# Optimization experiments

Measured on AMD Instinct MI355X. Metric: run time of the kernel, lower is better.

## Reference

```python
import jax, jax.numpy as jnp
import numpy as np

N_INST = 8  # max instance id; ids 1..N_INST, 0 = background
MESH_NORM = 1024.0  # from SegmantationLoss._meshgrid


def _meshgrid(H, W):
    y = jnp.arange(H, dtype=jnp.float32) / MESH_NORM
    x = jnp.arange(W, dtype=jnp.float32) / MESH_NORM
    return jnp.stack([jnp.broadcast_to(y[:, None], (H, W)),
                      jnp.broadcast_to(x[None, :], (H, W))], axis=0)  # [2,H,W]


def _lovasz_hinge_batch(logits, labels, delta=1.0):
    """logits, labels: [K,P] float. Returns [K] lovasz hinge losses."""
    signs = 2.0 * labels - 1.0
    errors = delta - logits * signs
    order = jnp.argsort(-errors, axis=1)  # descending
    es = jnp.take_along_axis(errors, order, axis=1)
    gs = jnp.take_along_axis(labels, order, axis=1)
    gts = gs.sum(axis=1, keepdims=True)
    intersection = gts - jnp.cumsum(gs, axis=1)
    union = gts + jnp.cumsum(1.0 - gs, axis=1)
    jac = 1.0 - intersection / union
    grad = jnp.concatenate([jac[:, :1], jac[:, 1:] - jac[:, :-1]], axis=1)
    return (jax.nn.relu(es) * grad).sum(axis=1)


def setup_inputs() -> dict:
    key = jax.random.key(0)
    k1, k2, k3, k4 = jax.random.split(key, 4)
    B, H, W = 4, 512, 1024
    x_vec = jax.random.normal(k1, (B, 2, H, W), dtype=jnp.float32)
    # small scale so psigma = exp(10*ppsigma) stays in a sane range
    x_sigma = jax.random.normal(k2, (B, 2, H, W), dtype=jnp.float32) * 0.03
    x_seed = jax.random.normal(k3, (B, 1, H, W), dtype=jnp.float32)
    t = jax.random.randint(k4, (B, H, W), 0, 9, dtype=jnp.int32)
    return {"x_vec": x_vec, "x_sigma": x_sigma, "x_seed": x_seed, "t": t}


def reference(x_vec, x_sigma, x_seed, t):
    B, _, H, W = x_vec.shape
    mesh = _meshgrid(H, W)

    emb = jnp.tanh(x_vec) + mesh[None]          # [B,2,H,W] spatial embedding
    ppsig = x_sigma                              # [B,2,H,W] pre-pseudo-sigma
    seed = jax.nn.sigmoid(x_seed)[:, 0]          # [B,H,W]

    ids = jnp.arange(1, N_INST + 1, dtype=t.dtype)
    mf = (t[None] == ids[:, None, None, None]).astype(jnp.float32)  # [N,B,H,W]
    cnt = mf.sum(axis=(2, 3))                    # [N,B]
    present = cnt > 0
    safe = jnp.maximum(cnt, 1.0)
    n_present = jnp.maximum(present.sum(axis=0).astype(jnp.float32), 1.0)  # [B]

    # per-instance masked means
    centroid = jnp.einsum('nbhw,bchw->nbc', mf, emb) / safe[..., None]    # [N,B,2]
    inst_pps = jnp.einsum('nbhw,bchw->nbc', mf, ppsig) / safe[..., None]  # [N,B,2]
    psigma = jnp.exp(10.0 * inst_pps)                                     # [N,B,2]

    # gaussian between pixel and instance embedding (l22n)
    diff2 = (emb[None] - centroid[..., None, None]) ** 2                  # [N,B,2,H,W]
    dist = (diff2 * psigma[..., None, None]).sum(axis=2)                  # [N,B,H,W]
    gauss = jnp.exp(-0.5 * dist)                                          # [N,B,H,W]

    # lovasz hinge per instance on logits 2*gauss - 1 over all pixels
    P = H * W
    lov = _lovasz_hinge_batch((2.0 * gauss - 1.0).reshape(N_INST * B, P),
                              mf.reshape(N_INST * B, P)).reshape(N_INST, B)
    lov = jnp.where(present, lov, 0.0)
    lovasz_loss = (lov.sum(axis=0) / n_present).mean()

    # sigma loss: pixel ppsigma -> detached instance mean ppsigma
    sd = (ppsig[None] - jax.lax.stop_gradient(inst_pps)[..., None, None]) ** 2
    sl = (sd.sum(axis=2) * mf).sum(axis=(2, 3)) / safe                    # [N,B]
    sl = jnp.where(present, sl, 0.0)
    sigma_loss = (sl.sum(axis=0) / n_present).mean()

    # seed loss: background -> 0, foreground -> detached gaussian
    bg = (t == 0).astype(jnp.float32)                                     # [B,H,W]
    bg_cnt = jnp.maximum(bg.sum(axis=(1, 2)), 1.0)
    bg_loss = ((seed ** 2) * bg).sum(axis=(1, 2)) / bg_cnt                # [B]
    fg = ((seed[None] - jax.lax.stop_gradient(gauss)) ** 2 * mf).sum(axis=(2, 3)) / safe
    fg = jnp.where(present, fg, 0.0)
    seed_loss = ((bg_loss + fg.sum(axis=0)) /
                 (1.0 + present.sum(axis=0).astype(jnp.float32))).mean()

    return lovasz_loss + sigma_loss + seed_loss
```

## Files before the change

kernel.cpp:

```cpp
#include <hip/hip_runtime.h>
#include <math.h>

#define B 4
#define H 512
#define W 1024
#define P (H*W)
#define NI 8
#define NSEG 32
#define NB 512
#define INV_BW ((float)NB/2.0f)
#define NSTRIP 256
#define STRIP_PX (P/NSTRIP)
#define K1B 128
#define K1PX (P/K1B)

#define D_CENY 0
#define D_CENX 32
#define D_PSY  64
#define D_PSX  96
#define D_CNT  128
#define D_SL   160
#define D_K4C  192
#define OFF_FGP 256
#define OFF_HIST (256 + 9*1024)
#define OFF_FOLD (OFF_HIST + NSEG*NSTRIP*NB)
#define OFF_PK1  OFF_HIST

__device__ __forceinline__ float fast_tanh(float x) {
    float e = __expf(2.0f * x);
    return 1.0f - 2.0f / (e + 1.0f);
}
__device__ __forceinline__ float fast_sigmoid(float x) {
    return 1.0f / (1.0f + __expf(-x));
}
template<int CTRL, int RM>
__device__ __forceinline__ float dpp_add(float x) {
    int y = __builtin_amdgcn_update_dpp(0, __float_as_int(x), CTRL, RM, 0xF, true);
    return x + __int_as_float(y);
}
__device__ __forceinline__ float wred(float x) {
    x = dpp_add<0x111, 0xF>(x);
    x = dpp_add<0x112, 0xF>(x);
    x = dpp_add<0x114, 0xF>(x);
    x = dpp_add<0x118, 0xF>(x);
    x = dpp_add<0x142, 0xA>(x);
    x = dpp_add<0x143, 0xC>(x);
    return x;
}

__global__ __launch_bounds__(256) void k1_stats(const float* __restrict__ xv,
                                                const float* __restrict__ xs,
                                                const int*  __restrict__ t,
                                                float* __restrict__ pk1) {
    const int b = blockIdx.y, bx = blockIdx.x, tid = threadIdx.x;
    const int lane = tid & 63, wid = tid >> 6;
    const float* xv_y = xv + (size_t)b*2*P;
    const float* xv_x = xv_y + P;
    const float* xs_y = xs + (size_t)b*2*P;
    const float* xs_x = xs_y + P;
    const int*   tb   = t + (size_t)b*P;

    float cnt[NI], sey[NI], sex[NI], sgy[NI], sgx[NI], sq[NI];
    #pragma unroll
    for (int n = 0; n < NI; ++n) { cnt[n]=0.f; sey[n]=0.f; sex[n]=0.f; sgy[n]=0.f; sgx[n]=0.f; sq[n]=0.f; }

    #pragma unroll
    for (int it = 0; it < 4; ++it) {
        int p0 = bx*K1PX + it*1024 + tid*4;
        float4 vy = *(const float4*)(xv_y + p0);
        float4 vx = *(const float4*)(xv_x + p0);
        float4 sy = *(const float4*)(xs_y + p0);
        float4 sx = *(const float4*)(xs_x + p0);
        int4   tt = *(const int4*)(tb + p0);
        #pragma unroll
        for (int j = 0; j < 4; ++j) {
            int pix = p0 + j;
            float ey = fast_tanh((&vy.x)[j]) + (float)(pix >> 10) * (1.0f/1024.0f);
            float ex = fast_tanh((&vx.x)[j]) + (float)(pix & 1023) * (1.0f/1024.0f);
            float gy = (&sy.x)[j], gx = (&sx.x)[j];
            int tv = (&tt.x)[j];
            float q = gy*gy + gx*gx;
            #pragma unroll
            for (int n = 0; n < NI; ++n) {
                float m = (tv == n+1) ? 1.0f : 0.0f;
                cnt[n] += m; sey[n] += m*ey; sex[n] += m*ex;
                sgy[n] += m*gy; sgx[n] += m*gx; sq[n] += m*q;
            }
        }
    }
    __shared__ float sw[4*64];
    #define RED48(val, slot) { float r_ = wred(val); if (lane == 63) sw[wid*64 + (slot)] = r_; }
    #pragma unroll
    for (int n = 0; n < NI; ++n) {
        RED48(cnt[n], n*6+0); RED48(sey[n], n*6+1); RED48(sex[n], n*6+2);
        RED48(sgy[n], n*6+3); RED48(sgx[n], n*6+4); RED48(sq[n],  n*6+5);
    }
    #undef RED48
    __syncthreads();
    if (tid < 48) {
        float s = sw[tid] + sw[64+tid] + sw[128+tid] + sw[192+tid];
        pk1[(size_t)(b*K1B + bx)*64 + tid] = s;
    }
}

__global__ __launch_bounds__(1024) void k2_finalize(float* __restrict__ wsf,
                                                    const float* __restrict__ pk1,
                                                    float* __restrict__ out) {
    const int tid = threadIdx.x;
    __shared__ float part[16*64];
    __shared__ float ssum[4*64];
    const int v = tid & 63, g = tid >> 6;
    const int b = g >> 2, c = g & 3;
    float acc = 0.f;
    const int jbase = b*K1B + c*32;
    #pragma unroll 8
    for (int i = 0; i < 32; ++i) acc += pk1[(size_t)(jbase + i)*64 + v];
    part[g*64 + v] = acc;
    __syncthreads();
    if (tid < 256) {
        int vb = tid & 63, bb = tid >> 6;
        ssum[bb*64+vb] = part[(bb*4+0)*64+vb] + part[(bb*4+1)*64+vb]
                       + part[(bb*4+2)*64+vb] + part[(bb*4+3)*64+vb];
    }
    __syncthreads();
    if (tid < NSEG) {
        int n = tid >> 2, bb = tid & 3;
        float cv  = ssum[bb*64 + n*6+0];
        float sey = ssum[bb*64 + n*6+1];
        float sex = ssum[bb*64 + n*6+2];
        float sgy = ssum[bb*64 + n*6+3];
        float sgx = ssum[bb*64 + n*6+4];
        float sq  = ssum[bb*64 + n*6+5];
        float safe = fmaxf(cv, 1.0f);
        float ipy = sgy/safe, ipx = sgx/safe;
        wsf[D_CENY+tid] = sey/safe;
        wsf[D_CENX+tid] = sex/safe;
        wsf[D_PSY+tid]  = expf(10.0f*ipy);
        wsf[D_PSX+tid]  = expf(10.0f*ipx);
        wsf[D_CNT+tid]  = cv;
        wsf[D_SL+tid]   = sq/safe - (ipy*ipy + ipx*ipx);
    } else if (tid < 64) {
        ((unsigned*)wsf)[D_K4C + (tid - 32)] = 0u;
    } else if (tid == 64) {
        out[0] = 0.f;
    }
}

__global__ __launch_bounds__(512) void k3_hist(const float* __restrict__ xv,
                                               const float* __restrict__ xseed,
                                               const int*  __restrict__ t,
                                               const float* __restrict__ wsf,
                                               unsigned* __restrict__ hist_g,
                                               float* __restrict__ fgp) {
    const int strip = blockIdx.x;
    const int b     = blockIdx.y;
    const int tid   = threadIdx.x;
    const int lane  = tid & 63;

    __shared__ unsigned hist[NI*NB];
    {
        uint4 z = {0u,0u,0u,0u};
        #pragma unroll
        for (int i = 0; i < 2; ++i) *((uint4*)hist + i*512 + tid) = z;
    }
    __shared__ float spar[4*NI];
    if (tid < 4*NI) {
        int n = tid & (NI-1), q = tid >> 3;
        spar[tid] = wsf[q*32 + n*B + b];
    }
    __syncthreads();

    float ceny[NI], cenx[NI], psy[NI], psx[NI], fgn[NI];
    #pragma unroll
    for (int n = 0; n < NI; ++n) {
        ceny[n] = spar[n]; cenx[n] = spar[NI+n];
        psy[n] = spar[2*NI+n]; psx[n] = spar[3*NI+n];
        fgn[n] = 0.f;
    }
    float bgq = 0.f;

    const float* xv_y = xv + (size_t)b*2*P;
    const float* xv_x = xv_y + P;
    const float* sdp  = xseed + (size_t)b*P;
    const int*   tb   = t + (size_t)b*P;

    {
        int p0 = strip * STRIP_PX + tid*4;
        float4 vy = *(const float4*)(xv_y + p0);
        float4 vx = *(const float4*)(xv_x + p0);
        float4 se = *(const float4*)(sdp + p0);
        int4   tt = *(const int4*)(tb + p0);
        #pragma unroll
        for (int j = 0; j < 4; ++j) {
            int pix = p0 + j;
            float ey = fast_tanh((&vy.x)[j]) + (float)(pix >> 10) * (1.0f/1024.0f);
            float ex = fast_tanh((&vx.x)[j]) + (float)(pix & 1023) * (1.0f/1024.0f);
            int tv = (&tt.x)[j];
            float gown = 0.f;
            #pragma unroll
            for (int n = 0; n < NI; ++n) {
                float dy = ey - ceny[n], dx = ex - cenx[n];
                float g = __expf(-0.5f * (psy[n]*dy*dy + psx[n]*dx*dx));
                bool lab = (tv == n+1);
                float err = lab ? (2.0f - 2.0f*g) : (2.0f*g);
                int key = (int)(err * INV_BW);
                key = key > (NB-1) ? (NB-1) : key;
                if (key > 0) atomicAdd(&hist[n*NB + key], lab ? 0x10000u : 1u);
                if (lab) gown = g;
            }
            float s = fast_sigmoid((&se.x)[j]);
            if (tv > 0) {
                float d = s - gown;
                float dd = d*d;
                #pragma unroll
                for (int n = 0; n < NI; ++n) fgn[n] += (tv == n+1) ? dd : 0.f;
            } else {
                bgq += s*s;
            }
        }
    }
    __syncthreads();
    #pragma unroll
    for (int i = 0; i < 2; ++i) {
        int lin = i*2048 + tid*4;
        int n = lin >> 9, key = lin & (NB-1);
        uint4 v = *(const uint4*)&hist[lin];
        *(uint4*)&hist_g[((size_t)((n*4 + b)*NSTRIP + strip))*NB + key] = v;
    }
    __shared__ float sfg[NI+1];
    if (tid < NI+1) sfg[tid] = 0.f;
    __syncthreads();
    #pragma unroll
    for (int n = 0; n < NI; ++n) {
        float r = wred(fgn[n]);
        if (lane == 63 && r != 0.f) atomicAdd(&sfg[n], r);
    }
    {
        float r = wred(bgq);
        if (lane == 63) atomicAdd(&sfg[NI], r);
    }
    __syncthreads();
    if (tid < NI+1) fgp[tid*1024 + b*NSTRIP + strip] = sfg[tid];
}

__global__ __launch_bounds__(256) void k4_fused(const unsigned* __restrict__ hist_g,
                                                unsigned* __restrict__ fold,
                                                float* __restrict__ wsf,
                                                const float* __restrict__ fgp,
                                                float* __restrict__ out) {
    const int q = blockIdx.x;
    const int seg = blockIdx.y;
    const int tid = threadIdx.x;

    #pragma unroll
    for (int h = 0; h < 2; ++h) {
        int key = h*256 + tid;
        const unsigned* src = hist_g + (size_t)(seg*NSTRIP + q*64)*NB + key;
        unsigned pos = 0u, neg = 0u;
        #pragma unroll 8
        for (int s = 0; s < 64; ++s) {
            unsigned v = src[(size_t)s*NB];
            pos += v >> 16; neg += v & 0xffffu;
        }
        fold[((size_t)q*NSEG + seg)*NB + key] = pos;
        fold[(size_t)4*NSEG*NB + ((size_t)q*NSEG + seg)*NB + key] = neg;
    }

    __shared__ unsigned slast;
    __syncthreads();
    if (tid == 0) {
        __threadfence();
        unsigned* cnt4 = (unsigned*)wsf + D_K4C;
        slast = __hip_atomic_fetch_add(&cnt4[seg], 1u, __ATOMIC_ACQ_REL,
                                       __HIP_MEMORY_SCOPE_AGENT);
    }
    __syncthreads();
    if (slast != 3u) return;
    __threadfence();

    const int n = seg >> 2, b = seg & 3;
    __shared__ float scnt[NSEG];
    __shared__ float sfr[256];
    __shared__ unsigned up[256], un[256];
    __shared__ double sdd[256];
    if (tid < NSEG) scnt[tid] = wsf[D_CNT + tid];
    __syncthreads();

    if (n == 0) {
        sfr[tid] = fgp[NI*1024 + b*NSTRIP + tid];
        __syncthreads();
        #pragma unroll
        for (int d = 128; d > 0; d >>= 1) {
            if (tid < d) sfr[tid] += sfr[tid + d];
            __syncthreads();
        }
        if (tid == 0) {
            float bgs = sfr[0];
            int np = 0; float ss = 0.f, csum = 0.f;
            for (int k = 0; k < NI; ++k) {
                float cv = scnt[k*4 + b];
                csum += cv;
                if (cv > 0.5f) { np++; ss += wsf[D_SL + k*4 + b]; }
            }
            float bgc = fmaxf((float)P - csum, 1.0f);
            float bgl = bgs / bgc;
            float npf = fmaxf((float)np, 1.0f);
            atomicAdd(out, (ss/npf + bgl/(1.0f + (float)np)) * (1.0f/(float)B));
        }
        __syncthreads();
    }

    const float G = scnt[seg];
    if (G < 0.5f) return;
    int npc = 0;
    #pragma unroll
    for (int k = 0; k < NI; ++k) npc += (scnt[k*4 + b] > 0.5f) ? 1 : 0;

    sfr[tid] = fgp[n*1024 + b*NSTRIP + tid];
    __syncthreads();
    #pragma unroll
    for (int d = 128; d > 0; d >>= 1) {
        if (tid < d) sfr[tid] += sfr[tid + d];
        __syncthreads();
    }
    const float FG = sfr[0];

    unsigned pos2[2] = {0u,0u}, neg2[2] = {0u,0u};
    #pragma unroll
    for (int qq = 0; qq < 4; ++qq) {
        uint2 pv = *((const uint2*)(fold + ((size_t)qq*NSEG + seg)*NB) + tid);
        uint2 nv = *((const uint2*)(fold + (size_t)4*NSEG*NB + ((size_t)qq*NSEG + seg)*NB) + tid);
        pos2[0] += pv.x; pos2[1] += pv.y;
        neg2[0] += nv.x; neg2[1] += nv.y;
    }
    unsigned tp = pos2[0] + pos2[1];
    unsigned tn = neg2[0] + neg2[1];

    up[tid] = tp; un[tid] = tn;
    __syncthreads();
    for (int d = 1; d < 256; d <<= 1) {
        unsigned ap = (tid + d < 256) ? up[tid + d] : 0u;
        unsigned an = (tid + d < 256) ? un[tid + d] : 0u;
        __syncthreads();
        up[tid] += ap; un[tid] += an;
        __syncthreads();
    }
    const unsigned TP = up[0], TN = un[0];
    const unsigned Gu = (unsigned)(G + 0.5f);
    const unsigned NEGu = (unsigned)P - Gu;
    unsigned cump = up[tid] - tp;
    unsigned cumn = un[tid] - tn;

    const double dG = (double)G;
    double acc = 0.0;
    #pragma unroll
    for (int j = 1; j >= 0; --j) {
        unsigned cp = pos2[j], cn = neg2[j];
        int key = tid*2 + j;
        if (tid == 0 && j == 0) { cp = Gu - TP; cn = NEGu - TN; }
        if (cp | cn) {
            unsigned ep = cump, en = cumn;
            unsigned epi = ep + cp, eni = en + cn;
            double jb = 1.0 - (dG - (double)ep)  / (dG + (double)en);
            double ja = 1.0 - (dG - (double)epi) / (dG + (double)eni);
            acc += (((double)key + 0.5) * (2.0/(double)NB)) * (ja - jb);
        }
        cump += cp; cumn += cn;
    }
    sdd[tid] = acc;
    __syncthreads();
    #pragma unroll
    for (int d = 128; d > 0; d >>= 1) {
        if (tid < d) sdd[tid] += sdd[tid + d];
        __syncthreads();
    }
    if (tid == 0) {
        float npf = fmaxf((float)npc, 1.0f);
        float val = (float)sdd[0] / (npf * (float)B)
                  + (FG / G) / ((1.0f + (float)npc) * (float)B);
        atomicAdd(out, val);
    }
}

extern "C" void kernel_launch(void* const* d_in, const int* in_sizes, int n_in,
                              void* d_out, int out_size, void* d_ws, size_t ws_size,
                              hipStream_t stream) {
    (void)in_sizes; (void)n_in; (void)out_size; (void)ws_size;
    const float* xv  = (const float*)d_in[0];
    const float* xs  = (const float*)d_in[1];
    const float* xsd = (const float*)d_in[2];
    const int*   t   = (const int*)d_in[3];
    float* wsf = (float*)d_ws;
    unsigned* hist_g = (unsigned*)d_ws + OFF_HIST;
    unsigned* fold   = (unsigned*)d_ws + OFF_FOLD;
    float* pk1 = wsf + OFF_PK1;
    float* fgp = wsf + OFF_FGP;
    float* out = (float*)d_out;

    k1_stats<<<dim3(K1B, B), 256, 0, stream>>>(xv, xs, t, pk1);
    k2_finalize<<<1, 1024, 0, stream>>>(wsf, pk1, out);
    k3_hist<<<dim3(NSTRIP, B), 512, 0, stream>>>(xv, xsd, t, wsf, hist_g, fgp);
    k4_fused<<<dim3(4, NSEG), 256, 0, stream>>>(hist_g, fold, wsf, fgp, out);
}
```

Measured before the change: 132.9 us.

## Halve Lovasz histogram bins and spread stats kernel over more blocks

Reduces the error histogram from 512 to 256 bins, which halves shared-memory zeroing, global histogram writes and the fold traffic, and lets each thread own exactly one bin in the final scan. It also splits the first statistics kernel into four times as many blocks, each handling one float4 group per thread, to raise parallelism, and moves the partials buffer to its own workspace region. The final segment block reuses its own folded counts from registers. The coarser binning lowers the resolution of the Lovasz approximation, which may change the loss value slightly.

```diff
diff --git a/kernel.cpp b/kernel.cpp
--- a/kernel.cpp
+++ b/kernel.cpp
@@ -7,11 +7,11 @@
 #define P (H*W)
 #define NI 8
 #define NSEG 32
-#define NB 512
+#define NB 256
 #define INV_BW ((float)NB/2.0f)
 #define NSTRIP 256
 #define STRIP_PX (P/NSTRIP)
-#define K1B 128
+#define K1B 512
 #define K1PX (P/K1B)
 
 #define D_CENY 0
@@ -22,9 +22,9 @@
 #define D_SL   160
 #define D_K4C  192
 #define OFF_FGP 256
-#define OFF_HIST (256 + 9*1024)
+#define OFF_HIST (OFF_FGP + 9*1024)
 #define OFF_FOLD (OFF_HIST + NSEG*NSTRIP*NB)
-#define OFF_PK1  OFF_HIST
+#define OFF_PK1  (OFF_FOLD + 8*NSEG*NB)
 
 __device__ __forceinline__ float fast_tanh(float x) {
     float e = __expf(2.0f * x);
@@ -64,28 +64,25 @@
     #pragma unroll
     for (int n = 0; n < NI; ++n) { cnt[n]=0.f; sey[n]=0.f; sex[n]=0.f; sgy[n]=0.f; sgx[n]=0.f; sq[n]=0.f; }
 
-    #pragma unroll
-    for (int it = 0; it < 4; ++it) {
-        int p0 = bx*K1PX + it*1024 + tid*4;
-        float4 vy = *(const float4*)(xv_y + p0);
-        float4 vx = *(const float4*)(xv_x + p0);
-        float4 sy = *(const float4*)(xs_y + p0);
-        float4 sx = *(const float4*)(xs_x + p0);
-        int4   tt = *(const int4*)(tb + p0);
+    int p0 = bx*K1PX + tid*4;
+    float4 vy = *(const float4*)(xv_y + p0);
+    float4 vx = *(const float4*)(xv_x + p0);
+    float4 sy = *(const float4*)(xs_y + p0);
+    float4 sx = *(const float4*)(xs_x + p0);
+    int4   tt = *(const int4*)(tb + p0);
+    #pragma unroll
+    for (int j = 0; j < 4; ++j) {
+        int pix = p0 + j;
+        float ey = fast_tanh((&vy.x)[j]) + (float)(pix >> 10) * (1.0f/1024.0f);
+        float ex = fast_tanh((&vx.x)[j]) + (float)(pix & 1023) * (1.0f/1024.0f);
+        float gy = (&sy.x)[j], gx = (&sx.x)[j];
+        int tv = (&tt.x)[j];
+        float q = gy*gy + gx*gx;
         #pragma unroll
-        for (int j = 0; j < 4; ++j) {
-            int pix = p0 + j;
-            float ey = fast_tanh((&vy.x)[j]) + (float)(pix >> 10) * (1.0f/1024.0f);
-            float ex = fast_tanh((&vx.x)[j]) + (float)(pix & 1023) * (1.0f/1024.0f);
-            float gy = (&sy.x)[j], gx = (&sx.x)[j];
-            int tv = (&tt.x)[j];
-            float q = gy*gy + gx*gx;
-            #pragma unroll
-            for (int n = 0; n < NI; ++n) {
-                float m = (tv == n+1) ? 1.0f : 0.0f;
-                cnt[n] += m; sey[n] += m*ey; sex[n] += m*ex;
-                sgy[n] += m*gy; sgx[n] += m*gx; sq[n] += m*q;
-            }
+        for (int n = 0; n < NI; ++n) {
+            float m = (tv == n+1) ? 1.0f : 0.0f;
+            cnt[n] += m; sey[n] += m*ey; sex[n] += m*ex;
+            sgy[n] += m*gy; sgx[n] += m*gx; sq[n] += m*q;
         }
     }
     __shared__ float sw[4*64];
@@ -112,9 +109,9 @@
     const int v = tid & 63, g = tid >> 6;
     const int b = g >> 2, c = g & 3;
     float acc = 0.f;
-    const int jbase = b*K1B + c*32;
+    const int jbase = b*K1B + c*128;
     #pragma unroll 8
-    for (int i = 0; i < 32; ++i) acc += pk1[(size_t)(jbase + i)*64 + v];
+    for (int i = 0; i < 128; ++i) acc += pk1[(size_t)(jbase + i)*64 + v];
     part[g*64 + v] = acc;
     __syncthreads();
     if (tid < 256) {
@@ -158,11 +155,7 @@
     const int lane  = tid & 63;
 
     __shared__ unsigned hist[NI*NB];
-    {
-        uint4 z = {0u,0u,0u,0u};
-        #pragma unroll
-        for (int i = 0; i < 2; ++i) *((uint4*)hist + i*512 + tid) = z;
-    }
+    *((uint4*)hist + tid) = (uint4){0u,0u,0u,0u};
     __shared__ float spar[4*NI];
     if (tid < 4*NI) {
         int n = tid & (NI-1), q = tid >> 3;
@@ -220,10 +213,9 @@
         }
     }
     __syncthreads();
-    #pragma unroll
-    for (int i = 0; i < 2; ++i) {
-        int lin = i*2048 + tid*4;
-        int n = lin >> 9, key = lin & (NB-1);
+    {
+        int lin = tid*4;
+        int n = lin >> 8, key = lin & (NB-1);
         uint4 v = *(const uint4*)&hist[lin];
         *(uint4*)&hist_g[((size_t)((n*4 + b)*NSTRIP + strip))*NB + key] = v;
     }
@@ -252,18 +244,18 @@
     const int seg = blockIdx.y;
     const int tid = threadIdx.x;
 
-    #pragma unroll
-    for (int h = 0; h < 2; ++h) {
-        int key = h*256 + tid;
-        const unsigned* src = hist_g + (size_t)(seg*NSTRIP + q*64)*NB + key;
+    unsigned posk, negk;
+    {
+        const unsigned* src = hist_g + (size_t)(seg*NSTRIP + q*64)*NB + tid;
         unsigned pos = 0u, neg = 0u;
         #pragma unroll 8
         for (int s = 0; s < 64; ++s) {
             unsigned v = src[(size_t)s*NB];
             pos += v >> 16; neg += v & 0xffffu;
         }
-        fold[((size_t)q*NSEG + seg)*NB + key] = pos;
-        fold[(size_t)4*NSEG*NB + ((size_t)q*NSEG + seg)*NB + key] = neg;
+        fold[((size_t)q*NSEG + seg)*NB + tid] = pos;
+        fold[(size_t)4*NSEG*NB + ((size_t)q*NSEG + seg)*NB + tid] = neg;
+        posk = pos; negk = neg;
     }
 
     __shared__ unsigned slast;
@@ -325,18 +317,15 @@
     }
     const float FG = sfr[0];
 
-    unsigned pos2[2] = {0u,0u}, neg2[2] = {0u,0u};
+    unsigned pos = posk, neg = negk;
     #pragma unroll
     for (int qq = 0; qq < 4; ++qq) {
-        uint2 pv = *((const uint2*)(fold + ((size_t)qq*NSEG + seg)*NB) + tid);
-        uint2 nv = *((const uint2*)(fold + (size_t)4*NSEG*NB + ((size_t)qq*NSEG + seg)*NB) + tid);
-        pos2[0] += pv.x; pos2[1] += pv.y;
-        neg2[0] += nv.x; neg2[1] += nv.y;
-    }
-    unsigned tp = pos2[0] + pos2[1];
-    unsigned tn = neg2[0] + neg2[1];
-
-    up[tid] = tp; un[tid] = tn;
+        if (qq == q) continue;
+        pos += fold[((size_t)qq*NSEG + seg)*NB + tid];
+        neg += fold[(size_t)4*NSEG*NB + ((size_t)qq*NSEG + seg)*NB + tid];
+    }
+
+    up[tid] = pos; un[tid] = neg;
     __syncthreads();
     for (int d = 1; d < 256; d <<= 1) {
         unsigned ap = (tid + d < 256) ? up[tid + d] : 0u;
@@ -348,24 +337,21 @@
     const unsigned TP = up[0], TN = un[0];
     const unsigned Gu = (unsigned)(G + 0.5f);
     const unsigned NEGu = (unsigned)P - Gu;
-    unsigned cump = up[tid] - tp;
-    unsigned cumn = un[tid] - tn;
+    unsigned cump = up[tid] - pos;
+    unsigned cumn = un[tid] - neg;
 
     const double dG = (double)G;
     double acc = 0.0;
-    #pragma unroll
-    for (int j = 1; j >= 0; --j) {
-        unsigned cp = pos2[j], cn = neg2[j];
-        int key = tid*2 + j;
-        if (tid == 0 && j == 0) { cp = Gu - TP; cn = NEGu - TN; }
+    {
+        unsigned cp = pos, cn = neg;
+        if (tid == 0) { cp = Gu - TP; cn = NEGu - TN; }
         if (cp | cn) {
             unsigned ep = cump, en = cumn;
             unsigned epi = ep + cp, eni = en + cn;
             double jb = 1.0 - (dG - (double)ep)  / (dG + (double)en);
             double ja = 1.0 - (dG - (double)epi) / (dG + (double)eni);
-            acc += (((double)key + 0.5) * (2.0/(double)NB)) * (ja - jb);
-        }
-        cump += cp; cumn += cn;
+            acc = (((double)tid + 0.5) * (2.0/(double)NB)) * (ja - jb);
+        }
     }
     sdd[tid] = acc;
     __syncthreads();
```

Result: no change. 132.6 us (-0.2%).
